# Kernel optimization log

Hardware: AMD Instinct MI355X
Metric: run time of the kernel (lower is better)

The kernel has to match this reference:

```python
import jax, jax.numpy as jnp
import numpy as np

IOU_THRESHOLD = 0.5


def setup_inputs() -> dict:
    key = jax.random.key(0)
    k1, k2, k3 = jax.random.split(key, 3)
    B, N = 4, 8192
    # valid boxes: top-left in [0,200), width/height in [1,51)
    xy = jax.random.uniform(k1, (B, N, 2), dtype=jnp.float32) * 200.0
    wh = jax.random.uniform(k2, (B, N, 2), dtype=jnp.float32) * 50.0 + 1.0
    boxes = jnp.concatenate([xy, xy + wh], axis=-1)  # [B,N,4] (x1,y1,x2,y2)
    scores = jax.random.uniform(k3, (B, N), dtype=jnp.float32)
    return {"boxes": boxes, "scores": scores}


def _soft_nms_single(boxes, scores):
    # boxes: [N,4], scores: [N]
    x1, y1, x2, y2 = boxes[:, 0], boxes[:, 1], boxes[:, 2], boxes[:, 3]
    inter_w = jnp.maximum(0.0, jnp.minimum(x2[:, None], x2[None, :]) - jnp.maximum(x1[:, None], x1[None, :]))
    inter_h = jnp.maximum(0.0, jnp.minimum(y2[:, None], y2[None, :]) - jnp.maximum(y1[:, None], y1[None, :]))
    inter = inter_w * inter_h  # [N,N]
    area = (x2 - x1) * (y2 - y1)  # [N]
    union = area[:, None] + area[None, :] - inter
    iou = inter / union  # [N,N]
    weight = jnp.exp(-iou / IOU_THRESHOLD)  # [N,N]
    adjusted = weight @ scores  # [N] : adjusted_scores[i] = sum_j w[i,j]*s[j]
    w = jax.nn.softmax(adjusted, axis=0)  # [N]
    return w @ boxes  # [4]


def reference(boxes, scores):
    return jax.vmap(_soft_nms_single)(boxes, scores)  # [B,4]
```

## Files before the change

kernel.cpp:

```cpp
#include <hip/hip_runtime.h>
#include <hip/hip_bf16.h>

#define BATCH   4
#define NBOX    8192
#define BLOCK   256
#define TSZ     256
#define NT      (NBOX / TSZ)
#define NPAIRS  (NT * (NT + 1) / 2)
#define NBINS   2048

__device__ __forceinline__ float bf2f(unsigned short u) {
    union { unsigned int i; float f; } c;
    c.i = ((unsigned int)u) << 16;
    return c.f;
}

__device__ __forceinline__ bool box_plausible(float x1, float y1, float x2, float y2) {
    bool ok = (x1 == x1) && (y1 == y1) && (x2 == x2) && (y2 == y2);
    ok = ok && fabsf(x1) < 1e4f && fabsf(y1) < 1e4f && fabsf(x2) < 1e4f && fabsf(y2) < 1e4f;
    ok = ok && x1 >= -1.0f && x1 <= 300.0f && y1 >= -1.0f && y1 <= 300.0f;
    const float w = x2 - x1, h = y2 - y1;
    ok = ok && w >= -0.1f && w <= 80.0f && h >= -0.1f && h <= 80.0f;
    return ok;
}

__device__ __forceinline__ bool wave_probe_is_f32(const void* boxes_raw) {
    const int lane = threadIdx.x & 63;
    const float* bf = (const float*)boxes_raw;
    const bool okf = box_plausible(bf[lane * 4 + 0], bf[lane * 4 + 1],
                                   bf[lane * 4 + 2], bf[lane * 4 + 3]);
    const unsigned short* bh = (const unsigned short*)boxes_raw;
    const bool okh = box_plausible(bf2f(bh[lane * 4 + 0]), bf2f(bh[lane * 4 + 1]),
                                   bf2f(bh[lane * 4 + 2]), bf2f(bh[lane * 4 + 3]));
    const unsigned long long mf = __ballot(okf);
    const unsigned long long mh = __ballot(okh);
    return __popcll(mf) >= __popcll(mh);
}

__device__ __forceinline__ float4 load_box(const void* boxes_raw, size_t idx, bool isf32) {
    if (isf32) {
        return reinterpret_cast<const float4*>(boxes_raw)[idx];
    } else {
        const ushort4 u = reinterpret_cast<const ushort4*>(boxes_raw)[idx];
        return make_float4(bf2f(u.x), bf2f(u.y), bf2f(u.z), bf2f(u.w));
    }
}

__device__ __forceinline__ float load_score(const void* scores_raw, size_t idx, bool isf32) {
    return isf32 ? ((const float*)scores_raw)[idx]
                 : bf2f(((const unsigned short*)scores_raw)[idx]);
}

#define CEXP (-2.8853900817779268f)

__device__ __forceinline__ float pair_weight(
    float ix1, float iy1, float ix2, float iy2, float iarea,
    const float4& bj, float jarea)
{
    float w = fminf(ix2, bj.z) - fmaxf(ix1, bj.x);
    float h = fminf(iy2, bj.w) - fmaxf(iy1, bj.y);
    w = fmaxf(w, 0.0f);
    h = fmaxf(h, 0.0f);
    const float inter = w * h;
    const float uni   = iarea + jarea - inter;
    const float arg   = (CEXP * inter) * __builtin_amdgcn_rcpf(uni);
    return __builtin_amdgcn_exp2f(arg);
}

__global__ __launch_bounds__(1024) void sort_kernel(
    const void* __restrict__ boxes_raw, const void* __restrict__ scores_raw,
    float4* __restrict__ sboxes, float* __restrict__ sscores,
    float* __restrict__ adj)
{
    __shared__ int hist[NBINS];
    __shared__ int wsum[1024];

    const int b   = blockIdx.x;
    const int tid = threadIdx.x;
    const bool isf32 = wave_probe_is_f32(boxes_raw);
    const size_t base = (size_t)b * NBOX;

    for (int i = tid; i < NBINS; i += 1024) hist[i] = 0;
#pragma unroll
    for (int k = 0; k < NBOX / 1024; k++) adj[base + k * 1024 + tid] = 0.0f;
    __syncthreads();

    float4 bx[8]; float sc[8]; int bin[8];
#pragma unroll
    for (int k = 0; k < 8; k++) {
        const int i = k * 1024 + tid;
        bx[k] = load_box(boxes_raw, base + i, isf32);
        sc[k] = load_score(scores_raw, base + i, isf32);
        int bb = (int)(bx[k].x * ((float)NBINS / 256.0f));
        bin[k] = min(NBINS - 1, max(0, bb));
        atomicAdd(&hist[bin[k]], 1);
    }
    __syncthreads();

    const int h0 = hist[2 * tid], h1 = hist[2 * tid + 1];
    const int s  = h0 + h1;
    wsum[tid] = s;
    __syncthreads();
    for (int off = 1; off < 1024; off <<= 1) {
        const int v = (tid >= off) ? wsum[tid - off] : 0;
        __syncthreads();
        wsum[tid] += v;
        __syncthreads();
    }
    const int ex = wsum[tid] - s;
    hist[2 * tid]     = ex;
    hist[2 * tid + 1] = ex + h0;
    __syncthreads();

#pragma unroll
    for (int k = 0; k < 8; k++) {
        const int pos = atomicAdd(&hist[bin[k]], 1);
        sboxes[base + pos]  = bx[k];
        sscores[base + pos] = sc[k];
    }
}

__global__ __launch_bounds__(BLOCK, 4) void soft_nms_adj_kernel(
    const float4* __restrict__ sboxes,
    const float* __restrict__ sscores,
    float* __restrict__ adj)
{
    __shared__ float4 sbox[TSZ];
    __shared__ float2 sas[TSZ];
    __shared__ float  srow[4][TSZ];
    __shared__ float  red[4][4];

    const int bid = blockIdx.x;
    const int b   = bid / NPAIRS;
    int p = bid % NPAIRS;
    int it = 0;
    while (p >= NT - it) { p -= NT - it; it++; }
    const int jt = it + p;

    const int tid  = threadIdx.x;
    const int lane = tid & 63;
    const int wv   = tid >> 6;
    const size_t base = (size_t)b * NBOX;

    float jmin, jmax;
    {
        const int jg = jt * TSZ + tid;
        const float4 uj = sboxes[base + jg];
        sbox[tid] = uj;
        sas[tid]  = make_float2((uj.z - uj.x) * (uj.w - uj.y), sscores[base + jg]);
        jmin = uj.x; jmax = uj.z;
    }

    float rx1[4], ry1[4], rx2[4], ry2[4], rar[4], rsc[4], accr[4];
#pragma unroll
    for (int k = 0; k < 4; k++) {
        const int ig = it * TSZ + k * 64 + lane;
        const float4 ui = sboxes[base + ig];
        rx1[k] = ui.x; ry1[k] = ui.y; rx2[k] = ui.z; ry2[k] = ui.w;
        rar[k] = (ui.z - ui.x) * (ui.w - ui.y);
        rsc[k] = sscores[base + ig];
        accr[k] = 0.0f;
    }

    float imin = fminf(fminf(rx1[0], rx1[1]), fminf(rx1[2], rx1[3]));
    float imax = fmaxf(fmaxf(rx2[0], rx2[1]), fmaxf(rx2[2], rx2[3]));
#pragma unroll
    for (int off = 32; off > 0; off >>= 1) {
        jmin = fminf(jmin, __shfl_down(jmin, off));
        jmax = fmaxf(jmax, __shfl_down(jmax, off));
        imin = fminf(imin, __shfl_down(imin, off));
        imax = fmaxf(imax, __shfl_down(imax, off));
    }
    if (lane == 0) {
        red[wv][0] = jmin; red[wv][1] = jmax; red[wv][2] = imin; red[wv][3] = imax;
    }
    __syncthreads();
    jmin = fminf(fminf(red[0][0], red[1][0]), fminf(red[2][0], red[3][0]));
    jmax = fmaxf(fmaxf(red[0][1], red[1][1]), fmaxf(red[2][1], red[3][1]));
    imin = fminf(fminf(red[0][2], red[1][2]), fminf(red[2][2], red[3][2]));
    imax = fmaxf(fmaxf(red[0][3], red[1][3]), fmaxf(red[2][3], red[3][3]));

    if ((imax < jmin) || (jmax < imin)) return;

    const int wvbase = wv * 64;

    if (it == jt) {
#pragma unroll 2
        for (int t = 0; t < 64; t++) {
            const int idx = wvbase + ((lane + t) & 63);
            const float4 bj = sbox[idx];
            const float2 as = sas[idx];
#pragma unroll
            for (int k = 0; k < 4; k++) {
                const float e = pair_weight(rx1[k], ry1[k], rx2[k], ry2[k], rar[k], bj, as.x);
                accr[k] = fmaf(e, as.y, accr[k]);
            }
        }
    } else {
        float accc = 0.0f;
#pragma unroll 2
        for (int t = 0; t < 64; t++) {
            const int idx = wvbase + ((lane + t) & 63);
            const float4 bj = sbox[idx];
            const float2 as = sas[idx];
            const float e0 = pair_weight(rx1[0], ry1[0], rx2[0], ry2[0], rar[0], bj, as.x);
            const float e1 = pair_weight(rx1[1], ry1[1], rx2[1], ry2[1], rar[1], bj, as.x);
            const float e2 = pair_weight(rx1[2], ry1[2], rx2[2], ry2[2], rar[2], bj, as.x);
            const float e3 = pair_weight(rx1[3], ry1[3], rx2[3], ry2[3], rar[3], bj, as.x);
            accr[0] = fmaf(e0, as.y, accr[0]);
            accr[1] = fmaf(e1, as.y, accr[1]);
            accr[2] = fmaf(e2, as.y, accr[2]);
            accr[3] = fmaf(e3, as.y, accr[3]);
            const float c = fmaf(e0, rsc[0], fmaf(e1, rsc[1], fmaf(e2, rsc[2], e3 * rsc[3])));
            accc += __shfl(c, (lane - t) & 63);
        }
        atomicAdd(&adj[base + jt * TSZ + wvbase + lane], accc);
    }

#pragma unroll
    for (int k = 0; k < 4; k++) srow[wv][k * 64 + lane] = accr[k];
    __syncthreads();
    {
        const float rs = srow[0][tid] + srow[1][tid] + srow[2][tid] + srow[3][tid];
        atomicAdd(&adj[base + it * TSZ + tid], rs);
    }
}

#define FBLK 1024
__global__ __launch_bounds__(FBLK) void soft_nms_finish_kernel(
    const float4* __restrict__ sboxes,
    const float* __restrict__ sscores,
    const float* __restrict__ adj,
    const void* __restrict__ boxes_raw,
    void* __restrict__ out)
{
    constexpr int K  = NBOX / FBLK;
    constexpr int NW = FBLK / 64;
    __shared__ float sminx[NT], smaxx[NT], ssumT[NT], scorr[NT];
    __shared__ float smax_[NW];
    __shared__ float sred[NW][5];

    const int b    = blockIdx.x;
    const int tid  = threadIdx.x;
    const int lane = tid & 63;
    const int wv   = tid >> 6;
    const size_t base = (size_t)b * NBOX;

    const bool isf32 = wave_probe_is_f32(boxes_raw);

#pragma unroll
    for (int tt = 0; tt < 2; tt++) {
        const int T = wv * 2 + tt;
        float mn = 1e30f, mx = -1e30f, sm = 0.0f;
#pragma unroll
        for (int q = 0; q < 4; q++) {
            const int i = T * TSZ + q * 64 + lane;
            const float4 u = sboxes[base + i];
            mn = fminf(mn, u.x);
            mx = fmaxf(mx, u.z);
            sm += sscores[base + i];
        }
#pragma unroll
        for (int off = 32; off > 0; off >>= 1) {
            mn = fminf(mn, __shfl_down(mn, off));
            mx = fmaxf(mx, __shfl_down(mx, off));
            sm += __shfl_down(sm, off);
        }
        if (lane == 0) { sminx[T] = mn; smaxx[T] = mx; ssumT[T] = sm; }
    }
    __syncthreads();
    if (tid < NT) {
        float c = 0.0f;
        for (int T2 = 0; T2 < NT; T2++) {
            const bool skip = (smaxx[tid] < sminx[T2]) || (smaxx[T2] < sminx[tid]);
            if (skip) c += ssumT[T2];
        }
        scorr[tid] = c;
    }
    __syncthreads();

    float av[K];
    float m = -3.4e38f;
#pragma unroll
    for (int k = 0; k < K; k++) {
        const int r = k * FBLK + tid;
        av[k] = adj[base + r] + scorr[r >> 8];
        m = fmaxf(m, av[k]);
    }
#pragma unroll
    for (int off = 32; off > 0; off >>= 1)
        m = fmaxf(m, __shfl_down(m, off));
    if (lane == 0) smax_[wv] = m;
    __syncthreads();
    float M = smax_[0];
#pragma unroll
    for (int w = 1; w < NW; w++) M = fmaxf(M, smax_[w]);

    const float L2E = 1.4426950408889634f;
    float es = 0.0f, s0 = 0.0f, s1 = 0.0f, s2 = 0.0f, s3 = 0.0f;
#pragma unroll
    for (int k = 0; k < K; k++) {
        const float e = __builtin_amdgcn_exp2f((av[k] - M) * L2E);
        const float4 u = sboxes[base + k * FBLK + tid];
        es += e;
        s0 += e * u.x;
        s1 += e * u.y;
        s2 += e * u.z;
        s3 += e * u.w;
    }
#pragma unroll
    for (int off = 32; off > 0; off >>= 1) {
        es += __shfl_down(es, off);
        s0 += __shfl_down(s0, off);
        s1 += __shfl_down(s1, off);
        s2 += __shfl_down(s2, off);
        s3 += __shfl_down(s3, off);
    }
    if (lane == 0) {
        sred[wv][0] = es; sred[wv][1] = s0; sred[wv][2] = s1;
        sred[wv][3] = s2; sred[wv][4] = s3;
    }
    __syncthreads();
    if (tid == 0) {
        float ES = 0.0f, o[4] = {0.0f, 0.0f, 0.0f, 0.0f};
#pragma unroll
        for (int w = 0; w < NW; w++) {
            ES   += sred[w][0];
            o[0] += sred[w][1];
            o[1] += sred[w][2];
            o[2] += sred[w][3];
            o[3] += sred[w][4];
        }
        const float inv = 1.0f / ES;
        if (isf32) {
            float* of = (float*)out;
            for (int c = 0; c < 4; c++) of[b * 4 + c] = o[c] * inv;
        } else {
            __hip_bfloat16* oh = (__hip_bfloat16*)out;
            for (int c = 0; c < 4; c++) oh[b * 4 + c] = __float2bfloat16(o[c] * inv);
        }
    }
}

extern "C" void kernel_launch(void* const* d_in, const int* in_sizes, int n_in,
                              void* d_out, int out_size, void* d_ws, size_t ws_size,
                              hipStream_t stream) {
    const void* boxes_raw  = d_in[0];
    const void* scores_raw = d_in[1];

    float4* sboxes  = (float4*)d_ws;
    float*  sscores = (float*)(sboxes + (size_t)BATCH * NBOX);
    float*  adj     = sscores + (size_t)BATCH * NBOX;

    sort_kernel<<<dim3(BATCH), dim3(1024), 0, stream>>>(
        boxes_raw, scores_raw, sboxes, sscores, adj);
    soft_nms_adj_kernel<<<dim3(BATCH * NPAIRS), dim3(BLOCK), 0, stream>>>(
        sboxes, sscores, adj);
    soft_nms_finish_kernel<<<dim3(BATCH), dim3(FBLK), 0, stream>>>(
        sboxes, sscores, adj, boxes_raw, d_out);
}
```

Baseline: 140.1 us.

## Precompute live tile-pair list and tile x-ranges in sort kernel

The sort kernel now records each tile's min x1 / max x2 and builds a compacted list of overlapping tile pairs with a count per batch. The adjacency kernel reads its pair from this list and exits immediately when the block index exceeds the count, instead of loading both tiles and doing a block reduction to find out the pair is disjoint. The shared-memory prefix scan is replaced with a wave-shuffle scan, and the finish kernel reuses the stored tile ranges. This adds shared atomics to the scatter loop and extra workspace.

```diff
diff --git a/kernel.cpp b/kernel.cpp
--- a/kernel.cpp
+++ b/kernel.cpp
@@ -70,17 +70,26 @@
 __global__ __launch_bounds__(1024) void sort_kernel(
     const void* __restrict__ boxes_raw, const void* __restrict__ scores_raw,
     float4* __restrict__ sboxes, float* __restrict__ sscores,
-    float* __restrict__ adj)
+    float* __restrict__ adj,
+    float* __restrict__ minxg, float* __restrict__ maxxg,
+    int* __restrict__ pairlist, int* __restrict__ count)
 {
     __shared__ int hist[NBINS];
-    __shared__ int wsum[1024];
-
-    const int b   = blockIdx.x;
-    const int tid = threadIdx.x;
+    __shared__ int wtot[16];
+    __shared__ int iminx[NT], imaxx[NT];
+    __shared__ int scnt;
+
+    const int b    = blockIdx.x;
+    const int tid  = threadIdx.x;
+    const int lane = tid & 63;
+    const int wv   = tid >> 6;
     const bool isf32 = wave_probe_is_f32(boxes_raw);
     const size_t base = (size_t)b * NBOX;
 
-    for (int i = tid; i < NBINS; i += 1024) hist[i] = 0;
+    hist[2 * tid]     = 0;
+    hist[2 * tid + 1] = 0;
+    if (tid < NT) { iminx[tid] = 0x7f800000; imaxx[tid] = 0; }
+    if (tid == 0) scnt = 0;
 #pragma unroll
     for (int k = 0; k < NBOX / 1024; k++) adj[base + k * 1024 + tid] = 0.0f;
     __syncthreads();
@@ -99,15 +108,25 @@
 
     const int h0 = hist[2 * tid], h1 = hist[2 * tid + 1];
     const int s  = h0 + h1;
-    wsum[tid] = s;
-    __syncthreads();
-    for (int off = 1; off < 1024; off <<= 1) {
-        const int v = (tid >= off) ? wsum[tid - off] : 0;
-        __syncthreads();
-        wsum[tid] += v;
-        __syncthreads();
-    }
-    const int ex = wsum[tid] - s;
+    int v = s;
+#pragma unroll
+    for (int d = 1; d < 64; d <<= 1) {
+        const int u = __shfl_up(v, d);
+        if (lane >= d) v += u;
+    }
+    if (lane == 63) wtot[wv] = v;
+    __syncthreads();
+    if (wv == 0 && lane < 16) {
+        int w = wtot[lane];
+#pragma unroll
+        for (int d = 1; d < 16; d <<= 1) {
+            const int u = __shfl_up(w, d);
+            if (lane >= d) w += u;
+        }
+        wtot[lane] = w;
+    }
+    __syncthreads();
+    const int ex = (wv > 0 ? wtot[wv - 1] : 0) + (v - s);
     hist[2 * tid]     = ex;
     hist[2 * tid + 1] = ex + h0;
     __syncthreads();
@@ -117,38 +136,60 @@
         const int pos = atomicAdd(&hist[bin[k]], 1);
         sboxes[base + pos]  = bx[k];
         sscores[base + pos] = sc[k];
-    }
+        const int T = pos >> 8;
+        atomicMin(&iminx[T], __float_as_int(bx[k].x));
+        atomicMax(&imaxx[T], __float_as_int(bx[k].z));
+    }
+    __syncthreads();
+
+    if (tid < NT) {
+        minxg[b * NT + tid] = __int_as_float(iminx[tid]);
+        maxxg[b * NT + tid] = __int_as_float(imaxx[tid]);
+    }
+    if (tid < NPAIRS) {
+        int p = tid, it = 0;
+        while (p >= NT - it) { p -= NT - it; it++; }
+        const int jt = it + p;
+        const float mi = __int_as_float(iminx[it]), Mi = __int_as_float(imaxx[it]);
+        const float mj = __int_as_float(iminx[jt]), Mj = __int_as_float(imaxx[jt]);
+        const bool live = !((Mi < mj) || (Mj < mi));
+        if (live) {
+            const int idx = atomicAdd(&scnt, 1);
+            pairlist[b * NPAIRS + idx] = (it << 8) | jt;
+        }
+    }
+    __syncthreads();
+    if (tid == 0) count[b] = scnt;
 }
 
 __global__ __launch_bounds__(BLOCK, 4) void soft_nms_adj_kernel(
     const float4* __restrict__ sboxes,
     const float* __restrict__ sscores,
+    const int* __restrict__ pairlist,
+    const int* __restrict__ count,
     float* __restrict__ adj)
 {
     __shared__ float4 sbox[TSZ];
     __shared__ float2 sas[TSZ];
     __shared__ float  srow[4][TSZ];
-    __shared__ float  red[4][4];
 
     const int bid = blockIdx.x;
     const int b   = bid / NPAIRS;
-    int p = bid % NPAIRS;
-    int it = 0;
-    while (p >= NT - it) { p -= NT - it; it++; }
-    const int jt = it + p;
+    const int p   = bid % NPAIRS;
+    if (p >= count[b]) return;
+    const int pr = pairlist[b * NPAIRS + p];
+    const int it = pr >> 8, jt = pr & 255;
 
     const int tid  = threadIdx.x;
     const int lane = tid & 63;
     const int wv   = tid >> 6;
     const size_t base = (size_t)b * NBOX;
 
-    float jmin, jmax;
     {
         const int jg = jt * TSZ + tid;
         const float4 uj = sboxes[base + jg];
         sbox[tid] = uj;
         sas[tid]  = make_float2((uj.z - uj.x) * (uj.w - uj.y), sscores[base + jg]);
-        jmin = uj.x; jmax = uj.z;
     }
 
     float rx1[4], ry1[4], rx2[4], ry2[4], rar[4], rsc[4], accr[4];
@@ -162,25 +203,7 @@
         accr[k] = 0.0f;
     }
 
-    float imin = fminf(fminf(rx1[0], rx1[1]), fminf(rx1[2], rx1[3]));
-    float imax = fmaxf(fmaxf(rx2[0], rx2[1]), fmaxf(rx2[2], rx2[3]));
-#pragma unroll
-    for (int off = 32; off > 0; off >>= 1) {
-        jmin = fminf(jmin, __shfl_down(jmin, off));
-        jmax = fmaxf(jmax, __shfl_down(jmax, off));
-        imin = fminf(imin, __shfl_down(imin, off));
-        imax = fmaxf(imax, __shfl_down(imax, off));
-    }
-    if (lane == 0) {
-        red[wv][0] = jmin; red[wv][1] = jmax; red[wv][2] = imin; red[wv][3] = imax;
-    }
-    __syncthreads();
-    jmin = fminf(fminf(red[0][0], red[1][0]), fminf(red[2][0], red[3][0]));
-    jmax = fmaxf(fmaxf(red[0][1], red[1][1]), fmaxf(red[2][1], red[3][1]));
-    imin = fminf(fminf(red[0][2], red[1][2]), fminf(red[2][2], red[3][2]));
-    imax = fmaxf(fmaxf(red[0][3], red[1][3]), fmaxf(red[2][3], red[3][3]));
-
-    if ((imax < jmin) || (jmax < imin)) return;
+    __syncthreads();
 
     const int wvbase = wv * 64;
 
@@ -231,6 +254,7 @@
     const float4* __restrict__ sboxes,
     const float* __restrict__ sscores,
     const float* __restrict__ adj,
+    const float* __restrict__ minxg, const float* __restrict__ maxxg,
     const void* __restrict__ boxes_raw,
     void* __restrict__ out)
 {
@@ -248,25 +272,19 @@
 
     const bool isf32 = wave_probe_is_f32(boxes_raw);
 
+    if (tid < NT) {
+        sminx[tid] = minxg[b * NT + tid];
+        smaxx[tid] = maxxg[b * NT + tid];
+    }
 #pragma unroll
     for (int tt = 0; tt < 2; tt++) {
         const int T = wv * 2 + tt;
-        float mn = 1e30f, mx = -1e30f, sm = 0.0f;
-#pragma unroll
-        for (int q = 0; q < 4; q++) {
-            const int i = T * TSZ + q * 64 + lane;
-            const float4 u = sboxes[base + i];
-            mn = fminf(mn, u.x);
-            mx = fmaxf(mx, u.z);
-            sm += sscores[base + i];
-        }
-#pragma unroll
-        for (int off = 32; off > 0; off >>= 1) {
-            mn = fminf(mn, __shfl_down(mn, off));
-            mx = fmaxf(mx, __shfl_down(mx, off));
-            sm += __shfl_down(sm, off);
-        }
-        if (lane == 0) { sminx[T] = mn; smaxx[T] = mx; ssumT[T] = sm; }
+        float sm = 0.0f;
+#pragma unroll
+        for (int q = 0; q < 4; q++) sm += sscores[base + T * TSZ + q * 64 + lane];
+#pragma unroll
+        for (int off = 32; off > 0; off >>= 1) sm += __shfl_down(sm, off);
+        if (lane == 0) ssumT[T] = sm;
     }
     __syncthreads();
     if (tid < NT) {
@@ -348,14 +366,19 @@
     const void* boxes_raw  = d_in[0];
     const void* scores_raw = d_in[1];
 
-    float4* sboxes  = (float4*)d_ws;
-    float*  sscores = (float*)(sboxes + (size_t)BATCH * NBOX);
-    float*  adj     = sscores + (size_t)BATCH * NBOX;
+    char* w = (char*)d_ws;
+    float4* sboxes   = (float4*)w;                     w += (size_t)BATCH * NBOX * 16;
+    float*  sscores  = (float*)w;                      w += (size_t)BATCH * NBOX * 4;
+    float*  adj      = (float*)w;                      w += (size_t)BATCH * NBOX * 4;
+    float*  minxg    = (float*)w;                      w += (size_t)BATCH * NT * 4;
+    float*  maxxg    = (float*)w;                      w += (size_t)BATCH * NT * 4;
+    int*    pairlist = (int*)w;                        w += (size_t)BATCH * NPAIRS * 4;
+    int*    count    = (int*)w;
 
     sort_kernel<<<dim3(BATCH), dim3(1024), 0, stream>>>(
-        boxes_raw, scores_raw, sboxes, sscores, adj);
+        boxes_raw, scores_raw, sboxes, sscores, adj, minxg, maxxg, pairlist, count);
     soft_nms_adj_kernel<<<dim3(BATCH * NPAIRS), dim3(BLOCK), 0, stream>>>(
-        sboxes, sscores, adj);
+        sboxes, sscores, pairlist, count, adj);
     soft_nms_finish_kernel<<<dim3(BATCH), dim3(FBLK), 0, stream>>>(
-        sboxes, sscores, adj, boxes_raw, d_out);
-}
+        sboxes, sscores, adj, minxg, maxxg, boxes_raw, d_out);
+}
```

New measurement: 121.7 us. -13.1%, faster.
